# Optimization experiments

Measured on AMD Instinct MI355X. Metric: run time of the kernel, lower is better.

Reference implementation:

```python
import jax, jax.numpy as jnp
import numpy as np

SEQ, BATCH, IN_DIM, HID = 512, 4096, 1, 30

def setup_inputs() -> dict:
    key = jax.random.key(0)
    ks = jax.random.split(key, 7)
    s = 1.0 / np.sqrt(HID)  # PyTorch RNN/Linear init scale
    X = jax.random.normal(ks[0], (SEQ, BATCH, IN_DIM), dtype=jnp.float32)
    W_ih = jax.random.uniform(ks[1], (HID, IN_DIM), jnp.float32, -s, s)
    W_hh = jax.random.uniform(ks[2], (HID, HID), jnp.float32, -s, s)
    b_ih = jax.random.uniform(ks[3], (HID,), jnp.float32, -s, s)
    b_hh = jax.random.uniform(ks[4], (HID,), jnp.float32, -s, s)
    W_out = jax.random.uniform(ks[5], (1, HID), jnp.float32, -s, s)
    b_out = jax.random.uniform(ks[6], (1,), jnp.float32, -s, s)
    return {"X": X, "W_ih": W_ih, "W_hh": W_hh, "b_ih": b_ih,
            "b_hh": b_hh, "W_out": W_out, "b_out": b_out}

def reference(X, W_ih, W_hh, b_ih, b_hh, W_out, b_out):
    # X: [S, B, 1]. Module transposes to batch_first [B, S, 1], runs tanh RNN,
    # applies Linear(30->1), transposes back -> [S, B, 1].
    S, B, _ = X.shape
    # Precompute input projection for all timesteps (input_size=1 -> cheap).
    x_proj = jnp.einsum('sbi,hi->sbh', X, W_ih) + b_ih + b_hh  # [S, B, H]
    h0 = jnp.zeros((B, W_hh.shape[0]), dtype=X.dtype)

    def step(h, xp):
        h_new = jnp.tanh(xp + h @ W_hh.T)
        return h_new, h_new

    _, hs = jax.lax.scan(step, h0, x_proj)  # hs: [S, B, H]
    y = jnp.einsum('sbh,oh->sbo', hs, W_out) + b_out  # [S, B, 1]
    return y
```

## Files before the change

kernel.cpp:

```cpp
#include <hip/hip_runtime.h>


#define SEQ 512
#define BATCH 4096
#define HID 30

template <int CTRL>
__device__ __forceinline__ float dpp_add_step(float x) {
  int moved = __builtin_amdgcn_update_dpp(0, __float_as_int(x), CTRL, 0xf, 0xf, true);
  return x + __int_as_float(moved);
}

__global__ __launch_bounds__(256, 2) void rnn_tanh_kernel(
    const float* __restrict__ X,
    const float* __restrict__ W_ih,
    const float* __restrict__ W_hh,
    const float* __restrict__ b_ih,
    const float* __restrict__ b_hh,
    const float* __restrict__ W_out,
    const float* __restrict__ b_out,
    float* __restrict__ Y)
{
  const int tid  = threadIdx.x;
  const int lane = tid & 31;
  const int g    = tid >> 5;
  const int gb   = blockIdx.x * 8 + g;

  __shared__ float hlds[8][32];

  float wih = 0.f, bsum = 0.f, wout = 0.f;
  float wrow[32];
#pragma unroll
  for (int j = 0; j < 32; ++j) wrow[j] = 0.f;
  if (lane < HID) {
    wih  = W_ih[lane];
    bsum = b_ih[lane] + b_hh[lane];
    wout = W_out[lane];
#pragma unroll
    for (int j = 0; j < HID; ++j) wrow[j] = W_hh[lane * HID + j];
  }
  const float bout = b_out[0];

  hlds[g][lane] = 0.f;
  const float* hp = &hlds[g][0];

  float4 hv0 = *reinterpret_cast<const float4*>(hp + 0);
  float4 hv1 = *reinterpret_cast<const float4*>(hp + 4);
  float4 hv2 = *reinterpret_cast<const float4*>(hp + 8);
  float4 hv3 = *reinterpret_cast<const float4*>(hp + 12);
  float4 hv4 = *reinterpret_cast<const float4*>(hp + 16);
  float4 hv5 = *reinterpret_cast<const float4*>(hp + 20);
  float4 hv6 = *reinterpret_cast<const float4*>(hp + 24);
  float4 hv7 = *reinterpret_cast<const float4*>(hp + 28);

  float x0 = X[0 * BATCH + gb];
  float x1 = X[1 * BATCH + gb];
  float x2 = X[2 * BATCH + gb];
  float x3 = X[3 * BATCH + gb];

  auto STEP = [&](int s, float& xreg) {
    float a0 = fmaf(xreg, wih, bsum);
    const int snext = (s + 4 < SEQ) ? s + 4 : SEQ - 1;
    xreg = X[snext * BATCH + gb];

    float a1 = 0.f, a2 = 0.f, a3 = 0.f;
    a0 = fmaf(wrow[0],  hv0.x, a0); a1 = fmaf(wrow[1],  hv0.y, a1);
    a2 = fmaf(wrow[2],  hv0.z, a2); a3 = fmaf(wrow[3],  hv0.w, a3);
    a0 = fmaf(wrow[4],  hv1.x, a0); a1 = fmaf(wrow[5],  hv1.y, a1);
    a2 = fmaf(wrow[6],  hv1.z, a2); a3 = fmaf(wrow[7],  hv1.w, a3);
    a0 = fmaf(wrow[8],  hv2.x, a0); a1 = fmaf(wrow[9],  hv2.y, a1);
    a2 = fmaf(wrow[10], hv2.z, a2); a3 = fmaf(wrow[11], hv2.w, a3);
    a0 = fmaf(wrow[12], hv3.x, a0); a1 = fmaf(wrow[13], hv3.y, a1);
    a2 = fmaf(wrow[14], hv3.z, a2); a3 = fmaf(wrow[15], hv3.w, a3);
    a0 = fmaf(wrow[16], hv4.x, a0); a1 = fmaf(wrow[17], hv4.y, a1);
    a2 = fmaf(wrow[18], hv4.z, a2); a3 = fmaf(wrow[19], hv4.w, a3);
    a0 = fmaf(wrow[20], hv5.x, a0); a1 = fmaf(wrow[21], hv5.y, a1);
    a2 = fmaf(wrow[22], hv5.z, a2); a3 = fmaf(wrow[23], hv5.w, a3);
    a0 = fmaf(wrow[24], hv6.x, a0); a1 = fmaf(wrow[25], hv6.y, a1);
    a2 = fmaf(wrow[26], hv6.z, a2); a3 = fmaf(wrow[27], hv6.w, a3);
    a0 = fmaf(wrow[28], hv7.x, a0); a1 = fmaf(wrow[29], hv7.y, a1);
    a2 = fmaf(wrow[30], hv7.z, a2); a3 = fmaf(wrow[31], hv7.w, a3);
    const float acc = (a0 + a1) + (a2 + a3);

    const float t = fminf(fmaxf(acc, -9.f), 9.f);
    const float e = __expf(2.f * t);
    const float h = fmaf(-2.f, __builtin_amdgcn_rcpf(e + 1.f), 1.f);

    hlds[g][lane] = h;
    hv0 = *reinterpret_cast<const float4*>(hp + 0);
    hv1 = *reinterpret_cast<const float4*>(hp + 4);
    hv2 = *reinterpret_cast<const float4*>(hp + 8);
    hv3 = *reinterpret_cast<const float4*>(hp + 12);
    hv4 = *reinterpret_cast<const float4*>(hp + 16);
    hv5 = *reinterpret_cast<const float4*>(hp + 20);
    hv6 = *reinterpret_cast<const float4*>(hp + 24);
    hv7 = *reinterpret_cast<const float4*>(hp + 28);

    float yp = h * wout;
    yp = dpp_add_step<0x111>(yp);
    yp = dpp_add_step<0x112>(yp);
    yp = dpp_add_step<0x114>(yp);
    yp = dpp_add_step<0x118>(yp);
    yp = dpp_add_step<0x142>(yp);
    if (lane == 31) Y[s * BATCH + gb] = yp + bout;
  };

  for (int s = 0; s < SEQ; s += 4) {
    STEP(s + 0, x0);
    STEP(s + 1, x1);
    STEP(s + 2, x2);
    STEP(s + 3, x3);
  }
}

extern "C" void kernel_launch(void* const* d_in, const int* in_sizes, int n_in,
                              void* d_out, int out_size, void* d_ws, size_t ws_size,
                              hipStream_t stream) {
  const float* X     = (const float*)d_in[0];
  const float* W_ih  = (const float*)d_in[1];
  const float* W_hh  = (const float*)d_in[2];
  const float* b_ih  = (const float*)d_in[3];
  const float* b_hh  = (const float*)d_in[4];
  const float* W_out = (const float*)d_in[5];
  const float* b_out = (const float*)d_in[6];
  float* Y = (float*)d_out;

  dim3 grid(BATCH / 8), block(256);
  rnn_tanh_kernel<<<grid, block, 0, stream>>>(X, W_ih, W_hh, b_ih, b_hh,
                                              W_out, b_out, Y);
}
```

Measured before the change: 124.1 us.

## Fold output projection into spare lane of recurrent matvec, drop DPP reduction

Lane 30, which was idle, now holds W_out as its weight row and b_out as its bias, so the recurrent FMA pass also yields the previous step's output and the per-step five-stage DPP reduction goes away. Output for step s-1 is written during step s, and one extra FMA pass after the loop produces the last output. Other changes: the weight row shrinks to 30 entries, the last LDS read becomes a float2, tanh uses fmed3 and exp2 builtins, and empty asm barriers keep the weights in VGPRs. Lane 30's x term stays zero because wih is zero there, but it still computes a tanh whose value lands in the unused slot 30 of shared memory.

```diff
diff --git a/kernel.cpp b/kernel.cpp
--- a/kernel.cpp
+++ b/kernel.cpp
@@ -4,12 +4,6 @@
 #define SEQ 512
 #define BATCH 4096
 #define HID 30
-
-template <int CTRL>
-__device__ __forceinline__ float dpp_add_step(float x) {
-  int moved = __builtin_amdgcn_update_dpp(0, __float_as_int(x), CTRL, 0xf, 0xf, true);
-  return x + __int_as_float(moved);
-}
 
 __global__ __launch_bounds__(256, 2) void rnn_tanh_kernel(
     const float* __restrict__ X,
@@ -28,18 +22,24 @@
 
   __shared__ float hlds[8][32];
 
-  float wih = 0.f, bsum = 0.f, wout = 0.f;
-  float wrow[32];
+  float wih = 0.f, bsum = 0.f;
+  float wrow[HID];
 #pragma unroll
-  for (int j = 0; j < 32; ++j) wrow[j] = 0.f;
+  for (int j = 0; j < HID; ++j) wrow[j] = 0.f;
   if (lane < HID) {
     wih  = W_ih[lane];
     bsum = b_ih[lane] + b_hh[lane];
-    wout = W_out[lane];
 #pragma unroll
     for (int j = 0; j < HID; ++j) wrow[j] = W_hh[lane * HID + j];
+  } else if (lane == HID) {
+    bsum = b_out[0];
+#pragma unroll
+    for (int j = 0; j < HID; ++j) wrow[j] = W_out[j];
   }
-  const float bout = b_out[0];
+#pragma unroll
+  for (int j = 0; j < HID; ++j) asm volatile("" : "+v"(wrow[j]));
+  asm volatile("" : "+v"(wih));
+  asm volatile("" : "+v"(bsum));
 
   hlds[g][lane] = 0.f;
   const float* hp = &hlds[g][0];
@@ -51,19 +51,15 @@
   float4 hv4 = *reinterpret_cast<const float4*>(hp + 16);
   float4 hv5 = *reinterpret_cast<const float4*>(hp + 20);
   float4 hv6 = *reinterpret_cast<const float4*>(hp + 24);
-  float4 hv7 = *reinterpret_cast<const float4*>(hp + 28);
+  float2 hv7 = *reinterpret_cast<const float2*>(hp + 28);
 
   float x0 = X[0 * BATCH + gb];
   float x1 = X[1 * BATCH + gb];
   float x2 = X[2 * BATCH + gb];
   float x3 = X[3 * BATCH + gb];
 
-  auto STEP = [&](int s, float& xreg) {
-    float a0 = fmaf(xreg, wih, bsum);
-    const int snext = (s + 4 < SEQ) ? s + 4 : SEQ - 1;
-    xreg = X[snext * BATCH + gb];
-
-    float a1 = 0.f, a2 = 0.f, a3 = 0.f;
+  auto FMA_PASS = [&](float init) -> float {
+    float a0 = init, a1 = 0.f, a2 = 0.f, a3 = 0.f;
     a0 = fmaf(wrow[0],  hv0.x, a0); a1 = fmaf(wrow[1],  hv0.y, a1);
     a2 = fmaf(wrow[2],  hv0.z, a2); a3 = fmaf(wrow[3],  hv0.w, a3);
     a0 = fmaf(wrow[4],  hv1.x, a0); a1 = fmaf(wrow[5],  hv1.y, a1);
@@ -79,11 +75,18 @@
     a0 = fmaf(wrow[24], hv6.x, a0); a1 = fmaf(wrow[25], hv6.y, a1);
     a2 = fmaf(wrow[26], hv6.z, a2); a3 = fmaf(wrow[27], hv6.w, a3);
     a0 = fmaf(wrow[28], hv7.x, a0); a1 = fmaf(wrow[29], hv7.y, a1);
-    a2 = fmaf(wrow[30], hv7.z, a2); a3 = fmaf(wrow[31], hv7.w, a3);
-    const float acc = (a0 + a1) + (a2 + a3);
+    return (a0 + a1) + (a2 + a3);
+  };
 
-    const float t = fminf(fmaxf(acc, -9.f), 9.f);
-    const float e = __expf(2.f * t);
+  auto STEP = [&](int s, float& xreg) {
+    float acc = FMA_PASS(fmaf(xreg, wih, bsum));
+    const int snext = (s + 4 < SEQ) ? s + 4 : SEQ - 1;
+    xreg = X[snext * BATCH + gb];
+
+    if (lane == HID && s != 0) Y[(s - 1) * BATCH + gb] = acc;
+
+    const float t = __builtin_amdgcn_fmed3f(acc, -9.f, 9.f);
+    const float e = __builtin_amdgcn_exp2f(t * 2.885390081777927f);
     const float h = fmaf(-2.f, __builtin_amdgcn_rcpf(e + 1.f), 1.f);
 
     hlds[g][lane] = h;
@@ -94,15 +97,7 @@
     hv4 = *reinterpret_cast<const float4*>(hp + 16);
     hv5 = *reinterpret_cast<const float4*>(hp + 20);
     hv6 = *reinterpret_cast<const float4*>(hp + 24);
-    hv7 = *reinterpret_cast<const float4*>(hp + 28);
-
-    float yp = h * wout;
-    yp = dpp_add_step<0x111>(yp);
-    yp = dpp_add_step<0x112>(yp);
-    yp = dpp_add_step<0x114>(yp);
-    yp = dpp_add_step<0x118>(yp);
-    yp = dpp_add_step<0x142>(yp);
-    if (lane == 31) Y[s * BATCH + gb] = yp + bout;
+    hv7 = *reinterpret_cast<const float2*>(hp + 28);
   };
 
   for (int s = 0; s < SEQ; s += 4) {
@@ -111,6 +106,9 @@
     STEP(s + 2, x2);
     STEP(s + 3, x3);
   }
+
+  const float ylast = FMA_PASS(bsum);
+  if (lane == HID) Y[(SEQ - 1) * BATCH + gb] = ylast;
 }
 
 extern "C" void kernel_launch(void* const* d_in, const int* in_sizes, int n_in,
```

Measured after the change: 100.5 us. 19.0% less time.
